# Kernel tuning notes

Measured on AMD Instinct MI355X. Metric: run time of the kernel, lower is better.

Reference implementation:

```python
import jax, jax.numpy as jnp
import numpy as np

B, S, D, H = 8, 1024, 1024, 16
HD = D // H  # 64


def setup_inputs() -> dict:
    key = jax.random.key(0)
    ks = jax.random.split(key, 10)
    s = 1.0 / np.sqrt(HD)
    x = jax.random.normal(ks[0], (B, S, D), dtype=jnp.float32)
    mask = jax.random.randint(ks[1], (B, S), 0, 2).astype(bool)  # True = padded
    # per-head q/k/v projections of SimpleAttention, stacked over heads
    Wq = jax.random.normal(ks[2], (H, HD, HD), dtype=jnp.float32) * s
    bq = jnp.zeros((H, HD), dtype=jnp.float32)
    Wk = jax.random.normal(ks[3], (H, HD, HD), dtype=jnp.float32) * s
    bk = jnp.zeros((H, HD), dtype=jnp.float32)
    Wv = jax.random.normal(ks[4], (H, HD, HD), dtype=jnp.float32) * s
    bv = jnp.zeros((H, HD), dtype=jnp.float32)
    # out_proj: Linear(dim, dim)
    Wo = jax.random.normal(ks[5], (D, D), dtype=jnp.float32) * (1.0 / np.sqrt(D))
    bo = jnp.zeros((D,), dtype=jnp.float32)
    return {"x": x, "mask": mask, "Wq": Wq, "bq": bq, "Wk": Wk, "bk": bk,
            "Wv": Wv, "bv": bv, "Wo": Wo, "bo": bo}


def reference(x, mask, Wq, bq, Wk, bk, Wv, bv, Wo, bo):
    b, s, d = x.shape
    xh = x.reshape(b, s, H, HD).transpose(0, 2, 1, 3)  # (b, h, s, hd)
    # per-head linear projections (batched over heads via einsum)
    q = jnp.einsum('bhsd,hde->bhse', xh, Wq) + bq[None, :, None, :]
    k = jnp.einsum('bhsd,hde->bhse', xh, Wk) + bk[None, :, None, :]
    v = jnp.einsum('bhsd,hde->bhse', xh, Wv) + bv[None, :, None, :]
    scale = 1.0 / jnp.sqrt(jnp.asarray(HD, dtype=x.dtype))
    scores = jnp.einsum('bhqd,bhkd->bhqk', q, k) * scale  # (b, h, s, s)
    # key-padding mask: True = padded -> -inf on key axis
    neg = jnp.asarray(jnp.finfo(x.dtype).min, dtype=x.dtype)
    scores = jnp.where(mask[:, None, None, :], neg, scores)
    attn = jax.nn.softmax(scores, axis=-1)
    out = jnp.einsum('bhqk,bhkd->bhqd', attn, v)  # (b, h, s, hd)
    concat = out.transpose(0, 2, 1, 3).reshape(b, s, d)
    # out_proj (dropout is identity in eval)
    return concat @ Wo.T + bo
```

## Files before the change

### kernel.cpp

```cpp
#include <hip/hip_runtime.h>
#include <float.h>

#define B_ 8
#define S_ 1024
#define D_ 1024
#define H_ 16
#define HD_ 64

typedef __attribute__((ext_vector_type(8))) _Float16 half8;
typedef __attribute__((ext_vector_type(4))) _Float16 half4;
typedef __attribute__((ext_vector_type(4))) float f32x4;

__device__ __forceinline__ void gld16(const void* g, void* l) {
  __builtin_amdgcn_global_load_lds(
      (const __attribute__((address_space(1))) void*)g,
      (__attribute__((address_space(3))) void*)l, 16, 0, 0);
}

__global__ __launch_bounds__(256) void prep_kernel(
    const float* __restrict__ Wq, const float* __restrict__ bq,
    const float* __restrict__ Wk, const float* __restrict__ bk,
    const float* __restrict__ Wv, const float* __restrict__ bv,
    const float* __restrict__ Wo, const void* __restrict__ mraw,
    _Float16* __restrict__ Wc, float* __restrict__ bs,
    _Float16* __restrict__ Wo16, float* __restrict__ maskadd) {
  const int bid = blockIdx.x;
  const int tid = threadIdx.x;
  if (bid < 768) {
    const int idx = bid * 256 + tid;
    const int d = idx & 63;
    const int e = (idx >> 6) & 63;
    const int t2 = idx >> 12;
    const int m = t2 % 3, h = t2 / 3;
    const int src = h * 4096 + d * 64 + e;
    float v = (m == 0) ? Wq[src] * 0.18033688f : (m == 1) ? Wk[src] : Wv[src];
    Wc[idx] = (_Float16)v;
    if (idx < 3072) {
      const int mm = idx >> 10, he = idx & 1023;
      float vv = (mm == 0) ? bq[he] * 0.18033688f : (mm == 1) ? bk[he] : bv[he];
      bs[idx] = vv;
    }
  } else if (bid < 800) {
    __shared__ int bad;
    if (tid == 0) bad = 0;
    __syncthreads();
    const unsigned int* mw = (const unsigned int*)mraw;
    int my = 0;
    for (int j = tid; j < 2048; j += 256) my |= (mw[j] & ~1u) ? 1 : 0;
    if (my) atomicOr(&bad, 1);
    __syncthreads();
    const int i = (bid - 768) * 256 + tid;
    const int f = bad;
    const int v = f ? (int)((const unsigned char*)mraw)[i] : ((const int*)mraw)[i];
    maskadd[i] = (v != 0) ? -FLT_MAX : 0.0f;
  } else {
    const int i = (bid - 800) * 256 + tid;
    Wo16[i] = (_Float16)Wo[i];
  }
}

__global__ __launch_bounds__(256) void qkv_kernel(
    const float* __restrict__ x, const _Float16* __restrict__ Wc,
    const float* __restrict__ bs,
    _Float16* __restrict__ q16, _Float16* __restrict__ k16, _Float16* __restrict__ vT16) {
  const int tile = blockIdx.x & 15;
  const int bh = blockIdx.x >> 4;
  const int b = bh >> 4, h = bh & 15;
  const int s0 = tile * 64;
  const int w = threadIdx.x >> 6, lane = threadIdx.x & 63;
  const int col = lane & 15, quad = lane >> 4;
  const int srow = s0 + w * 16 + col;

  const float* xr = x + ((size_t)(b * S_) + srow) * D_ + h * HD_;
  f32x4 x0a = *(const f32x4*)(xr + quad * 8);
  f32x4 x0b = *(const f32x4*)(xr + quad * 8 + 4);
  f32x4 x1a = *(const f32x4*)(xr + 32 + quad * 8);
  f32x4 x1b = *(const f32x4*)(xr + 32 + quad * 8 + 4);
  half8 Xf0, Xf1;
#pragma unroll
  for (int j = 0; j < 4; ++j) {
    Xf0[j] = (_Float16)x0a[j];
    Xf0[4 + j] = (_Float16)x0b[j];
    Xf1[j] = (_Float16)x1a[j];
    Xf1[4 + j] = (_Float16)x1b[j];
  }

  const _Float16* wbase = Wc + (size_t)h * 3 * 4096;
  const f32x4 z4 = {0.f, 0.f, 0.f, 0.f};
#pragma unroll
  for (int mm = 0; mm < 2; ++mm) {
    _Float16* outp = mm ? k16 : q16;
    const _Float16* wm = wbase + mm * 4096;
#pragma unroll
    for (int et = 0; et < 4; ++et) {
      const _Float16* wr = wm + (et * 16 + col) * 64;
      half8 W0 = *(const half8*)(wr + quad * 8);
      half8 W1 = *(const half8*)(wr + 32 + quad * 8);
      f32x4 c = __builtin_amdgcn_mfma_f32_16x16x32_f16(W0, Xf0, z4, 0, 0, 0);
      c = __builtin_amdgcn_mfma_f32_16x16x32_f16(W1, Xf1, c, 0, 0, 0);
      f32x4 bb = *(const f32x4*)(bs + mm * 1024 + h * 64 + et * 16 + quad * 4);
      half4 o;
#pragma unroll
      for (int r = 0; r < 4; ++r) o[r] = (_Float16)(c[r] + bb[r]);
      *(half4*)(outp + ((size_t)bh * S_ + srow) * HD_ + et * 16 + quad * 4) = o;
    }
  }
  {
    const _Float16* wm = wbase + 2 * 4096;
#pragma unroll
    for (int et = 0; et < 4; ++et) {
      const _Float16* wr = wm + (et * 16 + col) * 64;
      half8 W0 = *(const half8*)(wr + quad * 8);
      half8 W1 = *(const half8*)(wr + 32 + quad * 8);
      f32x4 c = __builtin_amdgcn_mfma_f32_16x16x32_f16(Xf0, W0, z4, 0, 0, 0);
      c = __builtin_amdgcn_mfma_f32_16x16x32_f16(Xf1, W1, c, 0, 0, 0);
      float bb = bs[2048 + h * 64 + et * 16 + col];
      half4 o;
#pragma unroll
      for (int r = 0; r < 4; ++r) o[r] = (_Float16)(c[r] + bb);
      *(half4*)(vT16 + ((size_t)bh * HD_ + et * 16 + col) * S_ + s0 + w * 16 + quad * 4) = o;
    }
  }
}

__global__ __launch_bounds__(256, 2) void attn_kernel(
    const _Float16* __restrict__ q, const _Float16* __restrict__ k,
    const _Float16* __restrict__ vT, const float* __restrict__ maskadd,
    _Float16* __restrict__ att) {
  __shared__ alignas(16) _Float16 Ks[2][64 * 64];
  __shared__ alignas(16) _Float16 Vs[2][64 * 64];
  const int bh = blockIdx.x & 127;
  const int qblk = blockIdx.x >> 7;
  const int b = bh >> 4, h = bh & 15;
  const int wv = threadIdx.x >> 6;
  const int lane = threadIdx.x & 63;
  const int quad = lane >> 4, col = lane & 15;
  const int c7 = col & 7;
  const int q0 = qblk * 256 + wv * 64;

  const _Float16* __restrict__ kb = k + (size_t)bh * S_ * HD_;
  const _Float16* __restrict__ vb = vT + (size_t)bh * HD_ * S_;
  const float* __restrict__ mrow = maskadd + b * S_;

  const int jj0 = wv * 128 + lane, jj1 = jj0 + 64;
  const int r0s = jj0 >> 3, r1s = jj1 >> 3;
  const int sg0 = (jj0 & 7) ^ (r0s & 7), sg1 = (jj1 & 7) ^ (r1s & 7);
  const int offK0 = r0s * 128 + sg0 * 16, offK1 = r1s * 128 + sg1 * 16;
  const int offV0 = r0s * 2048 + sg0 * 16, offV1 = r1s * 2048 + sg1 * 16;
  const int ldsb0 = wv * 1024, ldsb1 = wv * 1024 + 512;

  half8 Qf[4][2];
#pragma unroll
  for (int qt = 0; qt < 4; ++qt) {
    const _Float16* qrow = q + ((size_t)bh * S_ + q0 + qt * 16 + col) * HD_;
    Qf[qt][0] = *(const half8*)(qrow + quad * 8);
    Qf[qt][1] = *(const half8*)(qrow + 32 + quad * 8);
  }

  const f32x4 z4 = {0.f, 0.f, 0.f, 0.f};
  f32x4 O[4][4];
#pragma unroll
  for (int qt = 0; qt < 4; ++qt)
#pragma unroll
    for (int et = 0; et < 4; ++et) O[qt][et] = z4;
  float l[4] = {0.f, 0.f, 0.f, 0.f};

  {
    const char* kg = (const char*)kb;
    const char* vg = (const char*)vb;
    gld16(kg + offK0, &Ks[0][ldsb0]);
    gld16(kg + offK1, &Ks[0][ldsb1]);
    gld16(vg + offV0, &Vs[0][ldsb0]);
    gld16(vg + offV1, &Vs[0][ldsb1]);
  }
  int cur = 0;
  for (int c = 0; c < 16; ++c) {
    __syncthreads();
    if (c < 15) {
      const char* kg = (const char*)kb + (size_t)(c + 1) * 8192;
      const char* vg = (const char*)vb + (size_t)(c + 1) * 128;
      gld16(kg + offK0, &Ks[cur ^ 1][ldsb0]);
      gld16(kg + offK1, &Ks[cur ^ 1][ldsb1]);
      gld16(vg + offV0, &Vs[cur ^ 1][ldsb0]);
      gld16(vg + offV1, &Vs[cur ^ 1][ldsb1]);
    }
    const int kk0 = c * 64;
    const _Float16* Kb_ = &Ks[cur][0];
    const _Float16* Vb_ = &Vs[cur][0];
    f32x4 mkv[4];
#pragma unroll
    for (int kt = 0; kt < 4; ++kt) mkv[kt] = *(const f32x4*)(mrow + kk0 + kt * 16 + quad * 4);
    half8 Kf[4][2];
#pragma unroll
    for (int kt = 0; kt < 4; ++kt) {
      const int rb = (kt * 16 + col) * 64;
      Kf[kt][0] = *(const half8*)&Kb_[rb + ((quad) ^ c7) * 8];
      Kf[kt][1] = *(const half8*)&Kb_[rb + ((4 + quad) ^ c7) * 8];
    }
    half4 Vf[4][4];
#pragma unroll
    for (int kt = 0; kt < 4; ++kt) {
      const int sb = ((kt * 2 + (quad >> 1)) ^ c7) * 8 + (quad & 1) * 4;
#pragma unroll
      for (int et = 0; et < 4; ++et) Vf[kt][et] = *(const half4*)&Vb_[(et * 16 + col) * 64 + sb];
    }
#pragma unroll
    for (int qt = 0; qt < 4; ++qt) {
      f32x4 st[4];
#pragma unroll
      for (int kt = 0; kt < 4; ++kt) {
        f32x4 s = __builtin_amdgcn_mfma_f32_16x16x32_f16(Kf[kt][0], Qf[qt][0], mkv[kt], 0, 0, 0);
        st[kt] = __builtin_amdgcn_mfma_f32_16x16x32_f16(Kf[kt][1], Qf[qt][1], s, 0, 0, 0);
      }
      float p[16];
#pragma unroll
      for (int kt = 0; kt < 4; ++kt)
#pragma unroll
        for (int r = 0; r < 4; ++r) p[kt * 4 + r] = __builtin_amdgcn_exp2f(st[kt][r]);
      float s01 = (p[0] + p[1]) + (p[2] + p[3]);
      float s23 = (p[4] + p[5]) + (p[6] + p[7]);
      float s45 = (p[8] + p[9]) + (p[10] + p[11]);
      float s67 = (p[12] + p[13]) + (p[14] + p[15]);
      l[qt] += (s01 + s23) + (s45 + s67);
      half4 ph[4];
#pragma unroll
      for (int kt = 0; kt < 4; ++kt)
#pragma unroll
        for (int r = 0; r < 4; ++r) ph[kt][r] = (_Float16)p[kt * 4 + r];
#pragma unroll
      for (int et = 0; et < 4; ++et) {
        f32x4 o = O[qt][et];
#pragma unroll
        for (int kt = 0; kt < 4; ++kt)
          o = __builtin_amdgcn_mfma_f32_16x16x16f16(Vf[kt][et], ph[kt], o, 0, 0, 0);
        O[qt][et] = o;
      }
    }
    cur ^= 1;
  }
#pragma unroll
  for (int qt = 0; qt < 4; ++qt) {
    float lt = l[qt];
    lt += __shfl_xor(lt, 16);
    lt += __shfl_xor(lt, 32);
    const float inv = 1.0f / lt;
    _Float16* orow = att + ((size_t)(b * S_ + q0 + qt * 16 + col)) * D_ + h * HD_;
#pragma unroll
    for (int et = 0; et < 4; ++et) {
      half4 o;
#pragma unroll
      for (int r = 0; r < 4; ++r) o[r] = (_Float16)(O[qt][et][r] * inv);
      *(half4*)(orow + et * 16 + quad * 4) = o;
    }
  }
}

__global__ __launch_bounds__(256, 4) void outproj_kernel(
    const _Float16* __restrict__ A, const _Float16* __restrict__ Bw,
    const float* __restrict__ bo, float* __restrict__ C) {
  __shared__ alignas(16) _Float16 As[128 * 64];
  __shared__ alignas(16) _Float16 Bs[128 * 64];
  const int m0 = (int)(blockIdx.x >> 3) * 128;
  const int n0 = (int)(blockIdx.x & 7) * 128;
  const int t = threadIdx.x;
  const int lane = t & 63, wv = t >> 6;
  const int quad = lane >> 4, col = lane & 15;
  const int mw = (wv >> 1) * 64, nw = (wv & 1) * 64;

  int rowS[4], segS[4];
#pragma unroll
  for (int sweep = 0; sweep < 4; ++sweep) {
    const int s = sweep * 256 + wv * 64 + lane;
    rowS[sweep] = s >> 3;
    segS[sweep] = (s & 7) ^ (rowS[sweep] & 7);
  }

  f32x4 acc[16];
  const f32x4 z4 = {0.f, 0.f, 0.f, 0.f};
#pragma unroll
  for (int i = 0; i < 16; ++i) acc[i] = z4;

  for (int kt = 0; kt < 16; ++kt) {
#pragma unroll
    for (int sweep = 0; sweep < 4; ++sweep) {
      const int ldsbase = (sweep * 256 + wv * 64) * 8;
      gld16(A + (size_t)(m0 + rowS[sweep]) * D_ + kt * 64 + segS[sweep] * 8, &As[ldsbase]);
      gld16(Bw + (size_t)(n0 + rowS[sweep]) * D_ + kt * 64 + segS[sweep] * 8, &Bs[ldsbase]);
    }
    __syncthreads();
#pragma unroll
    for (int ks = 0; ks < 2; ++ks) {
      half8 aF[4], bF[4];
#pragma unroll
      for (int mt = 0; mt < 4; ++mt) {
        const int row = mw + mt * 16 + col;
        aF[mt] = *(const half8*)&As[row * 64 + (((ks * 4 + quad) ^ (row & 7)) * 8)];
      }
#pragma unroll
      for (int nt = 0; nt < 4; ++nt) {
        const int row = nw + nt * 16 + col;
        bF[nt] = *(const half8*)&Bs[row * 64 + (((ks * 4 + quad) ^ (row & 7)) * 8)];
      }
#pragma unroll
      for (int mt = 0; mt < 4; ++mt)
#pragma unroll
        for (int nt = 0; nt < 4; ++nt)
          acc[mt * 4 + nt] =
              __builtin_amdgcn_mfma_f32_16x16x32_f16(aF[mt], bF[nt], acc[mt * 4 + nt], 0, 0, 0);
    }
    __syncthreads();
  }
#pragma unroll
  for (int mt = 0; mt < 4; ++mt)
#pragma unroll
    for (int nt = 0; nt < 4; ++nt) {
      f32x4 a = acc[mt * 4 + nt];
      const int n = n0 + nw + nt * 16 + col;
      const float bb = bo[n];
#pragma unroll
      for (int r = 0; r < 4; ++r) {
        const int mrow = m0 + mw + mt * 16 + quad * 4 + r;
        C[(size_t)mrow * D_ + n] = a[r] + bb;
      }
    }
}

extern "C" void kernel_launch(void* const* d_in, const int* in_sizes, int n_in,
                              void* d_out, int out_size, void* d_ws, size_t ws_size,
                              hipStream_t stream) {
  const float* x  = (const float*)d_in[0];
  const float* Wq = (const float*)d_in[2];
  const float* bq = (const float*)d_in[3];
  const float* Wk = (const float*)d_in[4];
  const float* bk = (const float*)d_in[5];
  const float* Wv = (const float*)d_in[6];
  const float* bv = (const float*)d_in[7];
  const float* Wo = (const float*)d_in[8];
  const float* bo = (const float*)d_in[9];

  float* wsf     = (float*)d_ws;
  float* maskadd = wsf;
  const size_t NE = (size_t)B_ * H_ * S_ * HD_;
  _Float16* hws  = (_Float16*)(wsf + 16384);
  _Float16* q16  = hws;
  _Float16* k16  = q16 + NE;
  _Float16* vT16 = k16 + NE;
  _Float16* att16 = vT16 + NE;
  _Float16* Wo16 = att16 + NE;
  _Float16* Wc   = Wo16 + 1048576;
  float*    bs   = (float*)(Wc + 196608);

  prep_kernel<<<4896, 256, 0, stream>>>(Wq, bq, Wk, bk, Wv, bv, Wo, d_in[1],
                                        Wc, bs, Wo16, maskadd);
  qkv_kernel<<<B_ * H_ * (S_ / 64), 256, 0, stream>>>(x, Wc, bs, q16, k16, vT16);
  attn_kernel<<<B_ * H_ * (S_ / 256), 256, 0, stream>>>(q16, k16, vT16, maskadd, att16);
  outproj_kernel<<<(B_ * S_ / 128) * (D_ / 128), 256, 0, stream>>>(att16, Wo16, bo, (float*)d_out);
}
```

Baseline: 199.2 us.

## Triple-buffer K/V in attention, stage mask in LDS, use 16x16x32 MFMA for PV

Moves the attention kernel from double to triple buffering of K/V tiles, with an explicit vmcnt wait and a raw s_barrier so loads run two chunks ahead. The additive mask row is loaded once into shared memory instead of being read from global memory every chunk. The PV product now uses the 16x16x32 MFMA with concatenated V/P fragments, halving the MFMA instruction count, and s_setprio is raised around the MFMA blocks. More LDS per block may reduce occupancy, and the manual vmcnt counting is fragile if the compiler reorders memory operations.

```diff
diff --git a/kernel.cpp b/kernel.cpp
--- a/kernel.cpp
+++ b/kernel.cpp
@@ -127,8 +127,9 @@
     const _Float16* __restrict__ q, const _Float16* __restrict__ k,
     const _Float16* __restrict__ vT, const float* __restrict__ maskadd,
     _Float16* __restrict__ att) {
-  __shared__ alignas(16) _Float16 Ks[2][64 * 64];
-  __shared__ alignas(16) _Float16 Vs[2][64 * 64];
+  __shared__ alignas(16) _Float16 Ks[3][64 * 64];
+  __shared__ alignas(16) _Float16 Vs[3][64 * 64];
+  __shared__ alignas(16) float Ms[1024];
   const int bh = blockIdx.x & 127;
   const int qblk = blockIdx.x >> 7;
   const int b = bh >> 4, h = bh & 15;
@@ -165,6 +166,7 @@
     for (int et = 0; et < 4; ++et) O[qt][et] = z4;
   float l[4] = {0.f, 0.f, 0.f, 0.f};
 
+  gld16(mrow + wv * 256 + lane * 4, &Ms[wv * 256]);
   {
     const char* kg = (const char*)kb;
     const char* vg = (const char*)vb;
@@ -172,24 +174,36 @@
     gld16(kg + offK1, &Ks[0][ldsb1]);
     gld16(vg + offV0, &Vs[0][ldsb0]);
     gld16(vg + offV1, &Vs[0][ldsb1]);
-  }
+    kg += 8192; vg += 128;
+    gld16(kg + offK0, &Ks[1][ldsb0]);
+    gld16(kg + offK1, &Ks[1][ldsb1]);
+    gld16(vg + offV0, &Vs[1][ldsb0]);
+    gld16(vg + offV1, &Vs[1][ldsb1]);
+  }
+
   int cur = 0;
   for (int c = 0; c < 16; ++c) {
-    __syncthreads();
     if (c < 15) {
-      const char* kg = (const char*)kb + (size_t)(c + 1) * 8192;
-      const char* vg = (const char*)vb + (size_t)(c + 1) * 128;
-      gld16(kg + offK0, &Ks[cur ^ 1][ldsb0]);
-      gld16(kg + offK1, &Ks[cur ^ 1][ldsb1]);
-      gld16(vg + offV0, &Vs[cur ^ 1][ldsb0]);
-      gld16(vg + offV1, &Vs[cur ^ 1][ldsb1]);
-    }
-    const int kk0 = c * 64;
+      asm volatile("s_waitcnt vmcnt(4)" ::: "memory");
+    } else {
+      asm volatile("s_waitcnt vmcnt(0)" ::: "memory");
+    }
+    __builtin_amdgcn_s_barrier();
+    if (c < 14) {
+      int nb = cur + 2;
+      if (nb >= 3) nb -= 3;
+      const char* kg = (const char*)kb + (size_t)(c + 2) * 8192;
+      const char* vg = (const char*)vb + (size_t)(c + 2) * 128;
+      gld16(kg + offK0, &Ks[nb][ldsb0]);
+      gld16(kg + offK1, &Ks[nb][ldsb1]);
+      gld16(vg + offV0, &Vs[nb][ldsb0]);
+      gld16(vg + offV1, &Vs[nb][ldsb1]);
+    }
     const _Float16* Kb_ = &Ks[cur][0];
     const _Float16* Vb_ = &Vs[cur][0];
     f32x4 mkv[4];
 #pragma unroll
-    for (int kt = 0; kt < 4; ++kt) mkv[kt] = *(const f32x4*)(mrow + kk0 + kt * 16 + quad * 4);
+    for (int kt = 0; kt < 4; ++kt) mkv[kt] = *(const f32x4*)&Ms[c * 64 + kt * 16 + quad * 4];
     half8 Kf[4][2];
 #pragma unroll
     for (int kt = 0; kt < 4; ++kt) {
@@ -197,21 +211,35 @@
       Kf[kt][0] = *(const half8*)&Kb_[rb + ((quad) ^ c7) * 8];
       Kf[kt][1] = *(const half8*)&Kb_[rb + ((4 + quad) ^ c7) * 8];
     }
-    half4 Vf[4][4];
-#pragma unroll
-    for (int kt = 0; kt < 4; ++kt) {
-      const int sb = ((kt * 2 + (quad >> 1)) ^ c7) * 8 + (quad & 1) * 4;
-#pragma unroll
-      for (int et = 0; et < 4; ++et) Vf[kt][et] = *(const half4*)&Vb_[(et * 16 + col) * 64 + sb];
+    half8 Vf8[2][4];
+#pragma unroll
+    for (int pr = 0; pr < 2; ++pr) {
+      const int sb0 = (((pr * 2) * 2 + (quad >> 1)) ^ c7) * 8 + (quad & 1) * 4;
+      const int sb1 = (((pr * 2 + 1) * 2 + (quad >> 1)) ^ c7) * 8 + (quad & 1) * 4;
+#pragma unroll
+      for (int et = 0; et < 4; ++et) {
+        const int rb = (et * 16 + col) * 64;
+        half4 a = *(const half4*)&Vb_[rb + sb0];
+        half4 bq_ = *(const half4*)&Vb_[rb + sb1];
+        half8 t;
+#pragma unroll
+        for (int r = 0; r < 4; ++r) {
+          t[r] = a[r];
+          t[4 + r] = bq_[r];
+        }
+        Vf8[pr][et] = t;
+      }
     }
 #pragma unroll
     for (int qt = 0; qt < 4; ++qt) {
       f32x4 st[4];
+      __builtin_amdgcn_s_setprio(1);
 #pragma unroll
       for (int kt = 0; kt < 4; ++kt) {
         f32x4 s = __builtin_amdgcn_mfma_f32_16x16x32_f16(Kf[kt][0], Qf[qt][0], mkv[kt], 0, 0, 0);
         st[kt] = __builtin_amdgcn_mfma_f32_16x16x32_f16(Kf[kt][1], Qf[qt][1], s, 0, 0, 0);
       }
+      __builtin_amdgcn_s_setprio(0);
       float p[16];
 #pragma unroll
       for (int kt = 0; kt < 4; ++kt)
@@ -222,21 +250,23 @@
       float s45 = (p[8] + p[9]) + (p[10] + p[11]);
       float s67 = (p[12] + p[13]) + (p[14] + p[15]);
       l[qt] += (s01 + s23) + (s45 + s67);
-      half4 ph[4];
-#pragma unroll
-      for (int kt = 0; kt < 4; ++kt)
-#pragma unroll
-        for (int r = 0; r < 4; ++r) ph[kt][r] = (_Float16)p[kt * 4 + r];
+      half8 pp[2];
+#pragma unroll
+      for (int i = 0; i < 8; ++i) {
+        pp[0][i] = (_Float16)p[i];
+        pp[1][i] = (_Float16)p[8 + i];
+      }
+      __builtin_amdgcn_s_setprio(1);
 #pragma unroll
       for (int et = 0; et < 4; ++et) {
         f32x4 o = O[qt][et];
-#pragma unroll
-        for (int kt = 0; kt < 4; ++kt)
-          o = __builtin_amdgcn_mfma_f32_16x16x16f16(Vf[kt][et], ph[kt], o, 0, 0, 0);
+        o = __builtin_amdgcn_mfma_f32_16x16x32_f16(Vf8[0][et], pp[0], o, 0, 0, 0);
+        o = __builtin_amdgcn_mfma_f32_16x16x32_f16(Vf8[1][et], pp[1], o, 0, 0, 0);
         O[qt][et] = o;
       }
-    }
-    cur ^= 1;
+      __builtin_amdgcn_s_setprio(0);
+    }
+    cur = (cur == 2) ? 0 : cur + 1;
   }
 #pragma unroll
   for (int qt = 0; qt < 4; ++qt) {
```

Measured after the change: 199.7 us. About the same (+0.3%).

## Load K/V straight into registers with register double-buffering and wider PV MFMA

Applied to the files above, without the earlier changes.

The attention kernel no longer stages K and V tiles through shared memory with global_load_lds and per-chunk __syncthreads. Each wave now loads its K, V and mask fragments directly from global memory into registers, ping-ponging two K register buffers so the next chunk's loads are issued while the current chunk computes. The P·V product switches from four 16x16x16 MFMAs to two 16x16x32 MFMAs over a matching key permutation, and s_setprio is raised around the MFMA bursts. This removes LDS traffic and barriers, but every wave now fetches the full K/V from global/L2 separately, and register pressure rises under the 2-blocks-per-CU launch bound.

```diff
diff --git a/kernel.cpp b/kernel.cpp
--- a/kernel.cpp
+++ b/kernel.cpp
@@ -10,6 +10,11 @@
 typedef __attribute__((ext_vector_type(8))) _Float16 half8;
 typedef __attribute__((ext_vector_type(4))) _Float16 half4;
 typedef __attribute__((ext_vector_type(4))) float f32x4;
+
+typedef union {
+  half8 h8;
+  struct { half4 lo; half4 hi; } s;
+} h8u;
 
 __device__ __forceinline__ void gld16(const void* g, void* l) {
   __builtin_amdgcn_global_load_lds(
@@ -127,27 +132,21 @@
     const _Float16* __restrict__ q, const _Float16* __restrict__ k,
     const _Float16* __restrict__ vT, const float* __restrict__ maskadd,
     _Float16* __restrict__ att) {
-  __shared__ alignas(16) _Float16 Ks[2][64 * 64];
-  __shared__ alignas(16) _Float16 Vs[2][64 * 64];
   const int bh = blockIdx.x & 127;
   const int qblk = blockIdx.x >> 7;
   const int b = bh >> 4, h = bh & 15;
   const int wv = threadIdx.x >> 6;
   const int lane = threadIdx.x & 63;
   const int quad = lane >> 4, col = lane & 15;
-  const int c7 = col & 7;
   const int q0 = qblk * 256 + wv * 64;
 
   const _Float16* __restrict__ kb = k + (size_t)bh * S_ * HD_;
   const _Float16* __restrict__ vb = vT + (size_t)bh * HD_ * S_;
   const float* __restrict__ mrow = maskadd + b * S_;
 
-  const int jj0 = wv * 128 + lane, jj1 = jj0 + 64;
-  const int r0s = jj0 >> 3, r1s = jj1 >> 3;
-  const int sg0 = (jj0 & 7) ^ (r0s & 7), sg1 = (jj1 & 7) ^ (r1s & 7);
-  const int offK0 = r0s * 128 + sg0 * 16, offK1 = r1s * 128 + sg1 * 16;
-  const int offV0 = r0s * 2048 + sg0 * 16, offV1 = r1s * 2048 + sg1 * 16;
-  const int ldsb0 = wv * 1024, ldsb1 = wv * 1024 + 512;
+  const _Float16* kp = kb + col * 64 + quad * 8;
+  const int q4 = ((quad >> 1) * 8) + (quad & 1) * 4;
+  const _Float16* vp = vb + col * 1024 + q4;
 
   half8 Qf[4][2];
 #pragma unroll
@@ -157,61 +156,49 @@
     Qf[qt][1] = *(const half8*)(qrow + 32 + quad * 8);
   }
 
-  const f32x4 z4 = {0.f, 0.f, 0.f, 0.f};
   f32x4 O[4][4];
 #pragma unroll
   for (int qt = 0; qt < 4; ++qt)
 #pragma unroll
-    for (int et = 0; et < 4; ++et) O[qt][et] = z4;
+    for (int et = 0; et < 4; ++et) O[qt][et] = (f32x4){0.f, 0.f, 0.f, 0.f};
   float l[4] = {0.f, 0.f, 0.f, 0.f};
 
-  {
-    const char* kg = (const char*)kb;
-    const char* vg = (const char*)vb;
-    gld16(kg + offK0, &Ks[0][ldsb0]);
-    gld16(kg + offK1, &Ks[0][ldsb1]);
-    gld16(vg + offV0, &Vs[0][ldsb0]);
-    gld16(vg + offV1, &Vs[0][ldsb1]);
-  }
-  int cur = 0;
-  for (int c = 0; c < 16; ++c) {
-    __syncthreads();
-    if (c < 15) {
-      const char* kg = (const char*)kb + (size_t)(c + 1) * 8192;
-      const char* vg = (const char*)vb + (size_t)(c + 1) * 128;
-      gld16(kg + offK0, &Ks[cur ^ 1][ldsb0]);
-      gld16(kg + offK1, &Ks[cur ^ 1][ldsb1]);
-      gld16(vg + offV0, &Vs[cur ^ 1][ldsb0]);
-      gld16(vg + offV1, &Vs[cur ^ 1][ldsb1]);
-    }
-    const int kk0 = c * 64;
-    const _Float16* Kb_ = &Ks[cur][0];
-    const _Float16* Vb_ = &Vs[cur][0];
-    f32x4 mkv[4];
-#pragma unroll
-    for (int kt = 0; kt < 4; ++kt) mkv[kt] = *(const f32x4*)(mrow + kk0 + kt * 16 + quad * 4);
-    half8 Kf[4][2];
-#pragma unroll
-    for (int kt = 0; kt < 4; ++kt) {
-      const int rb = (kt * 16 + col) * 64;
-      Kf[kt][0] = *(const half8*)&Kb_[rb + ((quad) ^ c7) * 8];
-      Kf[kt][1] = *(const half8*)&Kb_[rb + ((4 + quad) ^ c7) * 8];
-    }
-    half4 Vf[4][4];
-#pragma unroll
-    for (int kt = 0; kt < 4; ++kt) {
-      const int sb = ((kt * 2 + (quad >> 1)) ^ c7) * 8 + (quad & 1) * 4;
-#pragma unroll
-      for (int et = 0; et < 4; ++et) Vf[kt][et] = *(const half4*)&Vb_[(et * 16 + col) * 64 + sb];
-    }
+  half8 KA[4][2], KB[4][2];
+  h8u V[2][4];
+  f32x4 mk[4];
+
+#define LOADK(DST, C)                                                      \
+  {                                                                        \
+    _Pragma("unroll") for (int kt = 0; kt < 4; ++kt) {                     \
+      DST[kt][0] = *(const half8*)(kp + (C) * 4096 + kt * 1024);           \
+      DST[kt][1] = *(const half8*)(kp + (C) * 4096 + kt * 1024 + 32);      \
+    }                                                                      \
+  }
+#define LOADV(C)                                                           \
+  {                                                                        \
+    _Pragma("unroll") for (int pr = 0; pr < 2; ++pr)                       \
+    _Pragma("unroll") for (int et = 0; et < 4; ++et) {                     \
+      V[pr][et].s.lo = *(const half4*)(vp + et * 16384 + (C) * 64 + pr * 32);        \
+      V[pr][et].s.hi = *(const half4*)(vp + et * 16384 + (C) * 64 + pr * 32 + 16);   \
+    }                                                                      \
+  }
+#define LOADM(C)                                                           \
+  {                                                                        \
+    _Pragma("unroll") for (int kt = 0; kt < 4; ++kt)                       \
+      mk[kt] = *(const f32x4*)(mrow + (C) * 64 + kt * 16 + quad * 4);      \
+  }
+
+  auto compute = [&](const half8 (&Kc)[4][2]) {
 #pragma unroll
     for (int qt = 0; qt < 4; ++qt) {
       f32x4 st[4];
+      __builtin_amdgcn_s_setprio(1);
 #pragma unroll
       for (int kt = 0; kt < 4; ++kt) {
-        f32x4 s = __builtin_amdgcn_mfma_f32_16x16x32_f16(Kf[kt][0], Qf[qt][0], mkv[kt], 0, 0, 0);
-        st[kt] = __builtin_amdgcn_mfma_f32_16x16x32_f16(Kf[kt][1], Qf[qt][1], s, 0, 0, 0);
-      }
+        f32x4 s = __builtin_amdgcn_mfma_f32_16x16x32_f16(Kc[kt][0], Qf[qt][0], mk[kt], 0, 0, 0);
+        st[kt] = __builtin_amdgcn_mfma_f32_16x16x32_f16(Kc[kt][1], Qf[qt][1], s, 0, 0, 0);
+      }
+      __builtin_amdgcn_s_setprio(0);
       float p[16];
 #pragma unroll
       for (int kt = 0; kt < 4; ++kt)
@@ -222,22 +209,44 @@
       float s45 = (p[8] + p[9]) + (p[10] + p[11]);
       float s67 = (p[12] + p[13]) + (p[14] + p[15]);
       l[qt] += (s01 + s23) + (s45 + s67);
-      half4 ph[4];
-#pragma unroll
-      for (int kt = 0; kt < 4; ++kt)
-#pragma unroll
-        for (int r = 0; r < 4; ++r) ph[kt][r] = (_Float16)p[kt * 4 + r];
+      half8 pp[2];
+#pragma unroll
+      for (int i = 0; i < 8; ++i) {
+        pp[0][i] = (_Float16)p[i];
+        pp[1][i] = (_Float16)p[8 + i];
+      }
+      __builtin_amdgcn_s_setprio(1);
 #pragma unroll
       for (int et = 0; et < 4; ++et) {
         f32x4 o = O[qt][et];
-#pragma unroll
-        for (int kt = 0; kt < 4; ++kt)
-          o = __builtin_amdgcn_mfma_f32_16x16x16f16(Vf[kt][et], ph[kt], o, 0, 0, 0);
+        o = __builtin_amdgcn_mfma_f32_16x16x32_f16(V[0][et].h8, pp[0], o, 0, 0, 0);
+        o = __builtin_amdgcn_mfma_f32_16x16x32_f16(V[1][et].h8, pp[1], o, 0, 0, 0);
         O[qt][et] = o;
       }
-    }
-    cur ^= 1;
-  }
+      __builtin_amdgcn_s_setprio(0);
+    }
+  };
+
+  LOADK(KA, 0);
+  LOADM(0);
+  LOADV(0);
+
+  for (int c = 0; c < 16; c += 2) {
+    LOADK(KB, c + 1);
+    compute(KA);
+    LOADM(c + 1);
+    LOADV(c + 1);
+    if (c + 2 < 16) LOADK(KA, c + 2);
+    compute(KB);
+    if (c + 2 < 16) {
+      LOADM(c + 2);
+      LOADV(c + 2);
+    }
+  }
+#undef LOADK
+#undef LOADV
+#undef LOADM
+
 #pragma unroll
   for (int qt = 0; qt < 4; ++qt) {
     float lt = l[qt];
```

After: 274.8 us. +38.0%, slower.

## Fuse QKV projection into attention kernel and remap outproj block order

Applied to the files above, without the earlier changes.

Removes the separate qkv kernel. The attention kernel now projects Q from x into LDS once, then projects each K/V chunk from x into the double-buffered LDS tiles before the chunk is used, replacing the async global-to-LDS loads. This avoids writing q/k/v in fp16 to memory and reading them back. The cost is recomputing the K/V projection in each of the 4 query blocks per head and running the projection work serially inside the loop instead of overlapping it with loads. The outproj block index mapping is also changed so that neighbouring blocks share tiles, which is meant to improve cache locality.

```diff
diff --git a/kernel.cpp b/kernel.cpp
--- a/kernel.cpp
+++ b/kernel.cpp
@@ -59,76 +59,13 @@
   }
 }
 
-__global__ __launch_bounds__(256) void qkv_kernel(
+__global__ __launch_bounds__(256, 2) void attn_kernel(
     const float* __restrict__ x, const _Float16* __restrict__ Wc,
-    const float* __restrict__ bs,
-    _Float16* __restrict__ q16, _Float16* __restrict__ k16, _Float16* __restrict__ vT16) {
-  const int tile = blockIdx.x & 15;
-  const int bh = blockIdx.x >> 4;
-  const int b = bh >> 4, h = bh & 15;
-  const int s0 = tile * 64;
-  const int w = threadIdx.x >> 6, lane = threadIdx.x & 63;
-  const int col = lane & 15, quad = lane >> 4;
-  const int srow = s0 + w * 16 + col;
-
-  const float* xr = x + ((size_t)(b * S_) + srow) * D_ + h * HD_;
-  f32x4 x0a = *(const f32x4*)(xr + quad * 8);
-  f32x4 x0b = *(const f32x4*)(xr + quad * 8 + 4);
-  f32x4 x1a = *(const f32x4*)(xr + 32 + quad * 8);
-  f32x4 x1b = *(const f32x4*)(xr + 32 + quad * 8 + 4);
-  half8 Xf0, Xf1;
-#pragma unroll
-  for (int j = 0; j < 4; ++j) {
-    Xf0[j] = (_Float16)x0a[j];
-    Xf0[4 + j] = (_Float16)x0b[j];
-    Xf1[j] = (_Float16)x1a[j];
-    Xf1[4 + j] = (_Float16)x1b[j];
-  }
-
-  const _Float16* wbase = Wc + (size_t)h * 3 * 4096;
-  const f32x4 z4 = {0.f, 0.f, 0.f, 0.f};
-#pragma unroll
-  for (int mm = 0; mm < 2; ++mm) {
-    _Float16* outp = mm ? k16 : q16;
-    const _Float16* wm = wbase + mm * 4096;
-#pragma unroll
-    for (int et = 0; et < 4; ++et) {
-      const _Float16* wr = wm + (et * 16 + col) * 64;
-      half8 W0 = *(const half8*)(wr + quad * 8);
-      half8 W1 = *(const half8*)(wr + 32 + quad * 8);
-      f32x4 c = __builtin_amdgcn_mfma_f32_16x16x32_f16(W0, Xf0, z4, 0, 0, 0);
-      c = __builtin_amdgcn_mfma_f32_16x16x32_f16(W1, Xf1, c, 0, 0, 0);
-      f32x4 bb = *(const f32x4*)(bs + mm * 1024 + h * 64 + et * 16 + quad * 4);
-      half4 o;
-#pragma unroll
-      for (int r = 0; r < 4; ++r) o[r] = (_Float16)(c[r] + bb[r]);
-      *(half4*)(outp + ((size_t)bh * S_ + srow) * HD_ + et * 16 + quad * 4) = o;
-    }
-  }
-  {
-    const _Float16* wm = wbase + 2 * 4096;
-#pragma unroll
-    for (int et = 0; et < 4; ++et) {
-      const _Float16* wr = wm + (et * 16 + col) * 64;
-      half8 W0 = *(const half8*)(wr + quad * 8);
-      half8 W1 = *(const half8*)(wr + 32 + quad * 8);
-      f32x4 c = __builtin_amdgcn_mfma_f32_16x16x32_f16(Xf0, W0, z4, 0, 0, 0);
-      c = __builtin_amdgcn_mfma_f32_16x16x32_f16(Xf1, W1, c, 0, 0, 0);
-      float bb = bs[2048 + h * 64 + et * 16 + col];
-      half4 o;
-#pragma unroll
-      for (int r = 0; r < 4; ++r) o[r] = (_Float16)(c[r] + bb);
-      *(half4*)(vT16 + ((size_t)bh * HD_ + et * 16 + col) * S_ + s0 + w * 16 + quad * 4) = o;
-    }
-  }
-}
-
-__global__ __launch_bounds__(256, 2) void attn_kernel(
-    const _Float16* __restrict__ q, const _Float16* __restrict__ k,
-    const _Float16* __restrict__ vT, const float* __restrict__ maskadd,
+    const float* __restrict__ bs, const float* __restrict__ maskadd,
     _Float16* __restrict__ att) {
   __shared__ alignas(16) _Float16 Ks[2][64 * 64];
   __shared__ alignas(16) _Float16 Vs[2][64 * 64];
+  __shared__ alignas(16) _Float16 Qstage[4 * 64 * 64];
   const int bh = blockIdx.x & 127;
   const int qblk = blockIdx.x >> 7;
   const int b = bh >> 4, h = bh & 15;
@@ -138,26 +75,67 @@
   const int c7 = col & 7;
   const int q0 = qblk * 256 + wv * 64;
 
-  const _Float16* __restrict__ kb = k + (size_t)bh * S_ * HD_;
-  const _Float16* __restrict__ vb = vT + (size_t)bh * HD_ * S_;
+  const float* __restrict__ xb = x + (size_t)b * S_ * D_ + h * HD_;
   const float* __restrict__ mrow = maskadd + b * S_;
-
-  const int jj0 = wv * 128 + lane, jj1 = jj0 + 64;
-  const int r0s = jj0 >> 3, r1s = jj1 >> 3;
-  const int sg0 = (jj0 & 7) ^ (r0s & 7), sg1 = (jj1 & 7) ^ (r1s & 7);
-  const int offK0 = r0s * 128 + sg0 * 16, offK1 = r1s * 128 + sg1 * 16;
-  const int offV0 = r0s * 2048 + sg0 * 16, offV1 = r1s * 2048 + sg1 * 16;
-  const int ldsb0 = wv * 1024, ldsb1 = wv * 1024 + 512;
-
+  const _Float16* wbase = Wc + (size_t)h * 3 * 4096;
+  const f32x4 z4 = {0.f, 0.f, 0.f, 0.f};
+
+  half8 WK[4][2], WV[4][2];
+  f32x4 bK[4];
+  f32x4 bV[4];
+#pragma unroll
+  for (int et = 0; et < 4; ++et) {
+    const _Float16* wrk = wbase + 4096 + (et * 16 + col) * 64;
+    WK[et][0] = *(const half8*)(wrk + quad * 8);
+    WK[et][1] = *(const half8*)(wrk + 32 + quad * 8);
+    const _Float16* wrv = wbase + 8192 + (et * 16 + col) * 64;
+    WV[et][0] = *(const half8*)(wrv + quad * 8);
+    WV[et][1] = *(const half8*)(wrv + 32 + quad * 8);
+    bK[et] = *(const f32x4*)(bs + 1024 + h * 64 + et * 16 + quad * 4);
+    const float bv_ = bs[2048 + h * 64 + et * 16 + col];
+    bV[et] = (f32x4){bv_, bv_, bv_, bv_};
+  }
+
+  {
+    _Float16* Qs = &Qstage[wv * 4096];
+#pragma unroll
+    for (int qt = 0; qt < 4; ++qt) {
+      const float* xr = xb + (size_t)(q0 + qt * 16 + col) * D_;
+      f32x4 a0 = *(const f32x4*)(xr + quad * 8);
+      f32x4 a1 = *(const f32x4*)(xr + quad * 8 + 4);
+      f32x4 a2 = *(const f32x4*)(xr + 32 + quad * 8);
+      f32x4 a3 = *(const f32x4*)(xr + 32 + quad * 8 + 4);
+      half8 X0, X1;
+#pragma unroll
+      for (int j = 0; j < 4; ++j) {
+        X0[j] = (_Float16)a0[j]; X0[4 + j] = (_Float16)a1[j];
+        X1[j] = (_Float16)a2[j]; X1[4 + j] = (_Float16)a3[j];
+      }
+#pragma unroll
+      for (int et = 0; et < 4; ++et) {
+        const _Float16* wrq = wbase + (et * 16 + col) * 64;
+        half8 Q0 = *(const half8*)(wrq + quad * 8);
+        half8 Q1 = *(const half8*)(wrq + 32 + quad * 8);
+        f32x4 bb = *(const f32x4*)(bs + h * 64 + et * 16 + quad * 4);
+        f32x4 c = __builtin_amdgcn_mfma_f32_16x16x32_f16(Q0, X0, bb, 0, 0, 0);
+        c = __builtin_amdgcn_mfma_f32_16x16x32_f16(Q1, X1, c, 0, 0, 0);
+        half4 o;
+#pragma unroll
+        for (int r = 0; r < 4; ++r) o[r] = (_Float16)c[r];
+        const int sg = (et * 2 + (quad >> 1)) ^ c7;
+        *(half4*)&Qs[(qt * 16 + col) * 64 + sg * 8 + (quad & 1) * 4] = o;
+      }
+    }
+  }
+  __syncthreads();
   half8 Qf[4][2];
 #pragma unroll
   for (int qt = 0; qt < 4; ++qt) {
-    const _Float16* qrow = q + ((size_t)bh * S_ + q0 + qt * 16 + col) * HD_;
-    Qf[qt][0] = *(const half8*)(qrow + quad * 8);
-    Qf[qt][1] = *(const half8*)(qrow + 32 + quad * 8);
-  }
-
-  const f32x4 z4 = {0.f, 0.f, 0.f, 0.f};
+    const int rb = wv * 4096 + (qt * 16 + col) * 64;
+    Qf[qt][0] = *(const half8*)&Qstage[rb + (quad ^ c7) * 8];
+    Qf[qt][1] = *(const half8*)&Qstage[rb + ((4 + quad) ^ c7) * 8];
+  }
+
   f32x4 O[4][4];
 #pragma unroll
   for (int qt = 0; qt < 4; ++qt)
@@ -165,28 +143,46 @@
     for (int et = 0; et < 4; ++et) O[qt][et] = z4;
   float l[4] = {0.f, 0.f, 0.f, 0.f};
 
-  {
-    const char* kg = (const char*)kb;
-    const char* vg = (const char*)vb;
-    gld16(kg + offK0, &Ks[0][ldsb0]);
-    gld16(kg + offK1, &Ks[0][ldsb1]);
-    gld16(vg + offV0, &Vs[0][ldsb0]);
-    gld16(vg + offV1, &Vs[0][ldsb1]);
-  }
-  int cur = 0;
+  auto project = [&](int c, int buf) {
+    const float* xr = xb + (size_t)(c * 64 + wv * 16 + col) * D_;
+    f32x4 a0 = *(const f32x4*)(xr + quad * 8);
+    f32x4 a1 = *(const f32x4*)(xr + quad * 8 + 4);
+    f32x4 a2 = *(const f32x4*)(xr + 32 + quad * 8);
+    f32x4 a3 = *(const f32x4*)(xr + 32 + quad * 8 + 4);
+    half8 X0, X1;
+#pragma unroll
+    for (int j = 0; j < 4; ++j) {
+      X0[j] = (_Float16)a0[j]; X0[4 + j] = (_Float16)a1[j];
+      X1[j] = (_Float16)a2[j]; X1[4 + j] = (_Float16)a3[j];
+    }
+    _Float16* KD = &Ks[buf][0];
+    _Float16* VD = &Vs[buf][0];
+#pragma unroll
+    for (int et = 0; et < 4; ++et) {
+      f32x4 ck = __builtin_amdgcn_mfma_f32_16x16x32_f16(WK[et][0], X0, bK[et], 0, 0, 0);
+      ck = __builtin_amdgcn_mfma_f32_16x16x32_f16(WK[et][1], X1, ck, 0, 0, 0);
+      half4 ok;
+#pragma unroll
+      for (int r = 0; r < 4; ++r) ok[r] = (_Float16)ck[r];
+      const int sgk = (et * 2 + (quad >> 1)) ^ c7;
+      *(half4*)&KD[(wv * 16 + col) * 64 + sgk * 8 + (quad & 1) * 4] = ok;
+      f32x4 cv = __builtin_amdgcn_mfma_f32_16x16x32_f16(X0, WV[et][0], bV[et], 0, 0, 0);
+      cv = __builtin_amdgcn_mfma_f32_16x16x32_f16(X1, WV[et][1], cv, 0, 0, 0);
+      half4 ov;
+#pragma unroll
+      for (int r = 0; r < 4; ++r) ov[r] = (_Float16)cv[r];
+      const int sgv = (wv * 2 + (quad >> 1)) ^ c7;
+      *(half4*)&VD[(et * 16 + col) * 64 + sgv * 8 + (quad & 1) * 4] = ov;
+    }
+  };
+
+  project(0, 0);
+  __syncthreads();
+
   for (int c = 0; c < 16; ++c) {
-    __syncthreads();
-    if (c < 15) {
-      const char* kg = (const char*)kb + (size_t)(c + 1) * 8192;
-      const char* vg = (const char*)vb + (size_t)(c + 1) * 128;
-      gld16(kg + offK0, &Ks[cur ^ 1][ldsb0]);
-      gld16(kg + offK1, &Ks[cur ^ 1][ldsb1]);
-      gld16(vg + offV0, &Vs[cur ^ 1][ldsb0]);
-      gld16(vg + offV1, &Vs[cur ^ 1][ldsb1]);
-    }
+    const _Float16* Kb_ = &Ks[c & 1][0];
+    const _Float16* Vb_ = &Vs[c & 1][0];
     const int kk0 = c * 64;
-    const _Float16* Kb_ = &Ks[cur][0];
-    const _Float16* Vb_ = &Vs[cur][0];
     f32x4 mkv[4];
 #pragma unroll
     for (int kt = 0; kt < 4; ++kt) mkv[kt] = *(const f32x4*)(mrow + kk0 + kt * 16 + quad * 4);
@@ -236,8 +232,10 @@
         O[qt][et] = o;
       }
     }
-    cur ^= 1;
-  }
+    if (c < 15) project(c + 1, (c + 1) & 1);
+    __syncthreads();
+  }
+
 #pragma unroll
   for (int qt = 0; qt < 4; ++qt) {
     float lt = l[qt];
@@ -260,8 +258,12 @@
     const float* __restrict__ bo, float* __restrict__ C) {
   __shared__ alignas(16) _Float16 As[128 * 64];
   __shared__ alignas(16) _Float16 Bs[128 * 64];
-  const int m0 = (int)(blockIdx.x >> 3) * 128;
-  const int n0 = (int)(blockIdx.x & 7) * 128;
+  const int x_ = blockIdx.x & 7;
+  const int t_ = blockIdx.x >> 3;
+  const int n_ = t_ & 7;
+  const int mlo = t_ >> 3;
+  const int m0 = (x_ * 8 + mlo) * 128;
+  const int n0 = n_ * 128;
   const int t = threadIdx.x;
   const int lane = t & 63, wv = t >> 6;
   const int quad = lane >> 4, col = lane & 15;
@@ -342,17 +344,13 @@
   float* maskadd = wsf;
   const size_t NE = (size_t)B_ * H_ * S_ * HD_;
   _Float16* hws  = (_Float16*)(wsf + 16384);
-  _Float16* q16  = hws;
-  _Float16* k16  = q16 + NE;
-  _Float16* vT16 = k16 + NE;
-  _Float16* att16 = vT16 + NE;
+  _Float16* att16 = hws;
   _Float16* Wo16 = att16 + NE;
   _Float16* Wc   = Wo16 + 1048576;
   float*    bs   = (float*)(Wc + 196608);
 
   prep_kernel<<<4896, 256, 0, stream>>>(Wq, bq, Wk, bk, Wv, bv, Wo, d_in[1],
                                         Wc, bs, Wo16, maskadd);
-  qkv_kernel<<<B_ * H_ * (S_ / 64), 256, 0, stream>>>(x, Wc, bs, q16, k16, vT16);
-  attn_kernel<<<B_ * H_ * (S_ / 256), 256, 0, stream>>>(q16, k16, vT16, maskadd, att16);
+  attn_kernel<<<B_ * H_ * (S_ / 256), 256, 0, stream>>>(x, Wc, bs, maskadd, att16);
   outproj_kernel<<<(B_ * S_ / 128) * (D_ / 128), 256, 0, stream>>>(att16, Wo16, bo, (float*)d_out);
 }
```

Measured after the change: 299.6 us. 50.4% more time.
